# Kernel tuning notes

Measured on AMD Instinct MI355X. Metric: run time of the kernel, lower is better.

## Reference

```python
import jax, jax.numpy as jnp
import numpy as np
import math

HIDDEN = 1024
HEADS = 16
HEAD_DIM = HIDDEN // HEADS
B, S = 4, 2048


def setup_inputs() -> dict:
    key = jax.random.key(0)
    ks = jax.random.split(key, 10)
    x = jax.random.normal(ks[0], (B, S, HIDDEN), dtype=jnp.float32)
    time_intervals = jax.random.uniform(ks[1], (B, S, S), dtype=jnp.float32)
    mask = jax.random.randint(ks[2], (B, 1, S, S), 0, 2, dtype=jnp.int32)
    scale = 1.0 / math.sqrt(HIDDEN)
    Wq = jax.random.normal(ks[3], (HIDDEN, HIDDEN), dtype=jnp.float32) * scale
    bq = jnp.zeros((HIDDEN,), dtype=jnp.float32)
    Wk = jax.random.normal(ks[4], (HIDDEN, HIDDEN), dtype=jnp.float32) * scale
    bk = jnp.zeros((HIDDEN,), dtype=jnp.float32)
    Wv = jax.random.normal(ks[5], (HIDDEN, HIDDEN), dtype=jnp.float32) * scale
    bv = jnp.zeros((HIDDEN,), dtype=jnp.float32)
    alpha = jnp.asarray(0.1, dtype=jnp.float32)
    return {"x": x, "time_intervals": time_intervals, "mask": mask,
            "Wq": Wq, "bq": bq, "Wk": Wk, "bk": bk, "Wv": Wv, "bv": bv,
            "alpha": alpha}


def reference(x, time_intervals, mask, Wq, bq, Wk, bk, Wv, bv, alpha):
    b, s, _ = x.shape
    # projections -> [b, heads, s, head_dim]
    def proj(W, bias):
        y = x @ W + bias
        return y.reshape(b, s, HEADS, HEAD_DIM).transpose(0, 2, 1, 3)
    Q = proj(Wq, bq)
    K = proj(Wk, bk)
    V = proj(Wv, bv)
    scores = jnp.einsum('bhqd,bhkd->bhqk', Q, K) / math.sqrt(HEAD_DIM)
    # additive time-decay bias, broadcast over heads
    scores = scores + (-jnp.abs(alpha)) * time_intervals[:, None, :, :]
    scores = jnp.where(mask == 0, jnp.float32(-1e9), scores)
    attn = jax.nn.softmax(scores, axis=-1)
    out = jnp.einsum('bhqk,bhkd->bhqd', attn, V)
    return out.transpose(0, 2, 1, 3).reshape(b, s, HIDDEN)
```

## Files before the change

### kernel.cpp

```cpp
#include <hip/hip_runtime.h>
#include <hip/hip_bf16.h>
#include <hip/hip_fp16.h>

#define BATCH 4
#define SEQ   2048
#define HID   1024
#define HEADS 16
#define HDIM  64
#define MROWS (BATCH * SEQ)
#define LOG2E 1.4426950408889634f
#define SCL   (LOG2E / 8.0f)

typedef _Float16 v8h __attribute__((ext_vector_type(8)));
typedef _Float16 v4h __attribute__((ext_vector_type(4)));
typedef _Float16 v2h __attribute__((ext_vector_type(2)));
typedef float    v4f __attribute__((ext_vector_type(4)));
typedef int      v4i __attribute__((ext_vector_type(4)));

#define MFMA16(a, b, c) __builtin_amdgcn_mfma_f32_16x16x32_f16((a), (b), (c), 0, 0, 0)

__device__ inline int pk2(float a, float b) {
    return __builtin_bit_cast(int, __builtin_amdgcn_cvt_pkrtz(a, b));
}

__global__ __launch_bounds__(256) void cvt_x(const float* __restrict__ x,
                                             _Float16* __restrict__ xb) {
    int i = blockIdx.x * 256 + threadIdx.x;
    const float4* xp = (const float4*)x;
    float4 a = xp[2 * i];
    float4 b = xp[2 * i + 1];
    v4i o;
    o[0] = pk2(a.x, a.y); o[1] = pk2(a.z, a.w);
    o[2] = pk2(b.x, b.y); o[3] = pk2(b.z, b.w);
    ((v4i*)xb)[i] = o;
}

__global__ __launch_bounds__(256) void transw(const float* __restrict__ W,
                                              _Float16* __restrict__ Wt) {
    __shared__ float t[32][33];
    int bx = blockIdx.x * 32, by = blockIdx.y * 32;
    int tx = threadIdx.x, ty = threadIdx.y;
#pragma unroll
    for (int i = 0; i < 4; i++)
        t[ty + i * 8][tx] = W[(size_t)(by + ty + i * 8) * HID + bx + tx];
    __syncthreads();
#pragma unroll
    for (int i = 0; i < 4; i++)
        Wt[(size_t)(bx + ty + i * 8) * HID + by + tx] = (_Float16)t[tx][ty + i * 8];
}

__global__ __launch_bounds__(256) void mkbias(const float* __restrict__ tiv,
                                              const int* __restrict__ msk,
                                              const float* __restrict__ alphap,
                                              _Float16* __restrict__ biasT) {
    __shared__ _Float16 L[16 * 264];
    const int b = blockIdx.z, Q16 = blockIdx.y, kc0 = blockIdx.x * 256;
    const int tid = threadIdx.x;
    const float ca = -fabsf(alphap[0]) * LOG2E;
    const int prow = tid >> 6;
    const int pcol = (tid & 63) * 4;
#pragma unroll
    for (int pi = 0; pi < 4; pi++) {
        int r = pi * 4 + prow;
        size_t g = ((size_t)b * SEQ + Q16 * 16 + r) * SEQ + kc0 + pcol;
        float4 tv = *(const float4*)(tiv + g);
        int4   mv = *(const int4*)(msk + g);
        float f0 = mv.x ? ca * tv.x : -57344.0f;
        float f1 = mv.y ? ca * tv.y : -57344.0f;
        float f2 = mv.z ? ca * tv.z : -57344.0f;
        float f3 = mv.w ? ca * tv.w : -57344.0f;
        int2 o; o.x = pk2(f0, f1); o.y = pk2(f2, f3);
        *(int2*)&L[r * 264 + pcol] = o;
    }
    __syncthreads();
    const int lane = tid & 63, tq = tid >> 6;
#pragma unroll
    for (int it = 0; it < 4; it++) {
        int K16i = it * 4 + tq;
        int kl = K16i * 16 + (lane >> 4) * 4;
        int qr = lane & 15;
        int2 v = *(const int2*)&L[qr * 264 + kl];
        size_t o = ((((size_t)b * 128 + (kc0 >> 4) + K16i) * 128 + Q16) * 64 + lane) * 4;
        *(int2*)&biasT[o] = v;
    }
}

#define LDT 72

__global__ __launch_bounds__(256) void gemm_qkv(
    const _Float16* __restrict__ xb, const _Float16* __restrict__ wt,
    const float* __restrict__ bq, const float* __restrict__ bk,
    const float* __restrict__ bv,
    _Float16* __restrict__ Qb, _Float16* __restrict__ Kb, _Float16* __restrict__ Vtb) {
    const int mode = blockIdx.z;
    const _Float16* w = wt + (size_t)mode * HID * HID;
    __shared__ _Float16 As[128 * LDT];
    __shared__ _Float16 Bs[128 * LDT];
    const int tid = threadIdx.x;
    const int wv = tid >> 6, lane = tid & 63;
    const int quad = lane >> 4, l15 = lane & 15;
    const int wr = wv >> 1, wc = wv & 1;
    const int m0 = blockIdx.y * 128;
    const int n0 = blockIdx.x * 128;

    v4f acc[4][4];
#pragma unroll
    for (int i = 0; i < 4; i++)
#pragma unroll
        for (int j = 0; j < 4; j++) acc[i][j] = (v4f){0.f, 0.f, 0.f, 0.f};

    const int sr = tid >> 3;
    const int sc = (tid & 7) * 8;
    const _Float16* Ag = xb + (size_t)m0 * HID;
    const _Float16* Bg = w + (size_t)n0 * HID;

    for (int k0 = 0; k0 < HID; k0 += 64) {
        __syncthreads();
#pragma unroll
        for (int i = 0; i < 4; i++) {
            int r = sr + i * 32;
            *(uint4*)&As[r * LDT + sc] = *(const uint4*)&Ag[(size_t)r * HID + k0 + sc];
            *(uint4*)&Bs[r * LDT + sc] = *(const uint4*)&Bg[(size_t)r * HID + k0 + sc];
        }
        __syncthreads();
#pragma unroll
        for (int kc = 0; kc < 2; kc++) {
            v8h af[4], bf[4];
#pragma unroll
            for (int t = 0; t < 4; t++) {
                af[t] = *(const v8h*)&As[(wr * 64 + t * 16 + l15) * LDT + kc * 32 + quad * 8];
                bf[t] = *(const v8h*)&Bs[(wc * 64 + t * 16 + l15) * LDT + kc * 32 + quad * 8];
            }
#pragma unroll
            for (int tm = 0; tm < 4; tm++)
#pragma unroll
                for (int tn = 0; tn < 4; tn++)
                    acc[tm][tn] = MFMA16(af[tm], bf[tn], acc[tm][tn]);
        }
    }

    const float* pb = (mode == 0) ? bq : (mode == 1 ? bk : bv);
#pragma unroll
    for (int tm = 0; tm < 4; tm++) {
#pragma unroll
        for (int tn = 0; tn < 4; tn++) {
            int n = n0 + wc * 64 + tn * 16 + l15;
            float bval = pb[n];
            int h = n >> 6, d = n & 63;
#pragma unroll
            for (int r = 0; r < 4; r++) {
                int m = m0 + wr * 64 + tm * 16 + quad * 4 + r;
                int b = m >> 11, s = m & 2047;
                _Float16 hv = (_Float16)(acc[tm][tn][r] + bval);
                if (mode == 2) {
                    Vtb[(((size_t)(b * HEADS + h) * HDIM + d) * SEQ) + s] = hv;
                } else {
                    _Float16* dst = (mode == 0) ? Qb : Kb;
                    dst[((size_t)(b * HEADS + h) * SEQ + s) * HDIM + d] = hv;
                }
            }
        }
    }
}

__global__ __launch_bounds__(256, 4) void attn(
    const _Float16* __restrict__ Qb, const _Float16* __restrict__ Kb,
    const _Float16* __restrict__ Vtb, const _Float16* __restrict__ biasT,
    float* __restrict__ out) {
    const int bh = blockIdx.y;
    const int b = bh >> 4, h = bh & 15;
    const int qt = blockIdx.x;
    const int tid = threadIdx.x;
    const int wv = tid >> 6, lane = tid & 63;
    const int quad = lane >> 4, l15 = lane & 15;

    __shared__ _Float16 Ks[64 * LDT];
    __shared__ _Float16 Vs[64 * LDT];

    const int q0 = qt * 128 + wv * 32;
    const int Q16a = q0 >> 4;

    const _Float16* Qp = Qb + (size_t)(b * HEADS + h) * SEQ * HDIM;
    const _Float16* Kp = Kb + (size_t)(b * HEADS + h) * SEQ * HDIM;
    const _Float16* Vp = Vtb + (size_t)(b * HEADS + h) * HDIM * SEQ;
    const _Float16* Bbase = biasT + (size_t)b * 128 * 128 * 64 * 4;

    v8h qf[2][2];
#pragma unroll
    for (int tm = 0; tm < 2; tm++)
#pragma unroll
        for (int kc = 0; kc < 2; kc++)
            qf[tm][kc] = *(const v8h*)&Qp[(size_t)(q0 + tm * 16 + l15) * HDIM + kc * 32 + quad * 8];

    v4f oacc[2][4];
#pragma unroll
    for (int i = 0; i < 2; i++)
#pragma unroll
        for (int j = 0; j < 4; j++) oacc[i][j] = (v4f){0.f, 0.f, 0.f, 0.f};
    float lsum[2] = {0.f, 0.f};

    const int addrA = ((quad & 1) * 32 + l15) * 4;
    const int addrB = addrA + 64;
    const bool hiq = (quad >= 2);

    for (int kt = 0; kt < SEQ / 64; kt++) {
        const int key0 = kt * 64;
        int2 bld[4][2];
#pragma unroll
        for (int nt = 0; nt < 4; nt++)
#pragma unroll
            for (int tm = 0; tm < 2; tm++)
                bld[nt][tm] = *(const int2*)&Bbase[((((size_t)(key0 >> 4) + nt) * 128 + Q16a + tm) * 64 + lane) * 4];

        __syncthreads();
#pragma unroll
        for (int i = 0; i < 2; i++) {
            int idx = tid + 256 * i;
            int rr = idx >> 3, cc = (idx & 7) * 8;
            *(uint4*)&Ks[rr * LDT + cc] = *(const uint4*)&Kp[(size_t)(key0 + rr) * HDIM + cc];
            *(uint4*)&Vs[rr * LDT + cc] = *(const uint4*)&Vp[(size_t)rr * SEQ + key0 + cc];
        }
        __syncthreads();

        v4f sacc[4][2];
#pragma unroll
        for (int i = 0; i < 4; i++)
#pragma unroll
            for (int j = 0; j < 2; j++) sacc[i][j] = (v4f){0.f, 0.f, 0.f, 0.f};
#pragma unroll
        for (int kc = 0; kc < 2; kc++) {
            v8h kfr[4];
#pragma unroll
            for (int nt = 0; nt < 4; nt++)
                kfr[nt] = *(const v8h*)&Ks[(nt * 16 + l15) * LDT + kc * 32 + quad * 8];
#pragma unroll
            for (int nt = 0; nt < 4; nt++)
#pragma unroll
                for (int tm = 0; tm < 2; tm++)
                    sacc[nt][tm] = MFMA16(kfr[nt], qf[tm][kc], sacc[nt][tm]);
        }

        int pk[4][2][2];
#pragma unroll
        for (int nt = 0; nt < 4; nt++)
#pragma unroll
            for (int tm = 0; tm < 2; tm++) {
                v4h bv = __builtin_bit_cast(v4h, bld[nt][tm]);
                float p0 = __builtin_amdgcn_exp2f(sacc[nt][tm][0] * SCL + (float)bv[0]);
                float p1 = __builtin_amdgcn_exp2f(sacc[nt][tm][1] * SCL + (float)bv[1]);
                float p2 = __builtin_amdgcn_exp2f(sacc[nt][tm][2] * SCL + (float)bv[2]);
                float p3 = __builtin_amdgcn_exp2f(sacc[nt][tm][3] * SCL + (float)bv[3]);
                lsum[tm] += (p0 + p1) + (p2 + p3);
                pk[nt][tm][0] = pk2(p0, p1);
                pk[nt][tm][1] = pk2(p2, p3);
            }

        v8h pf[2][2];
#pragma unroll
        for (int kc = 0; kc < 2; kc++)
#pragma unroll
            for (int tm = 0; tm < 2; tm++) {
                int d0l = __builtin_amdgcn_ds_bpermute(addrA, pk[kc * 2][tm][0]);
                int d0h = __builtin_amdgcn_ds_bpermute(addrA, pk[kc * 2 + 1][tm][0]);
                int d1l = __builtin_amdgcn_ds_bpermute(addrA, pk[kc * 2][tm][1]);
                int d1h = __builtin_amdgcn_ds_bpermute(addrA, pk[kc * 2 + 1][tm][1]);
                int d2l = __builtin_amdgcn_ds_bpermute(addrB, pk[kc * 2][tm][0]);
                int d2h = __builtin_amdgcn_ds_bpermute(addrB, pk[kc * 2 + 1][tm][0]);
                int d3l = __builtin_amdgcn_ds_bpermute(addrB, pk[kc * 2][tm][1]);
                int d3h = __builtin_amdgcn_ds_bpermute(addrB, pk[kc * 2 + 1][tm][1]);
                v4i dw;
                dw[0] = hiq ? d0h : d0l;
                dw[1] = hiq ? d1h : d1l;
                dw[2] = hiq ? d2h : d2l;
                dw[3] = hiq ? d3h : d3l;
                pf[kc][tm] = __builtin_bit_cast(v8h, dw);
            }

#pragma unroll
        for (int kc = 0; kc < 2; kc++) {
            v8h vfr[4];
#pragma unroll
            for (int nt = 0; nt < 4; nt++)
                vfr[nt] = *(const v8h*)&Vs[(nt * 16 + l15) * LDT + kc * 32 + quad * 8];
#pragma unroll
            for (int tm = 0; tm < 2; tm++)
#pragma unroll
                for (int nt = 0; nt < 4; nt++)
                    oacc[tm][nt] = MFMA16(pf[kc][tm], vfr[nt], oacc[tm][nt]);
        }
    }

#pragma unroll
    for (int tm = 0; tm < 2; tm++) {
        float lt = lsum[tm];
        lt += __shfl_xor(lt, 16);
        lt += __shfl_xor(lt, 32);
        float inv[4];
#pragma unroll
        for (int r = 0; r < 4; r++)
            inv[r] = 1.0f / __shfl(lt, quad * 4 + r);
#pragma unroll
        for (int nt = 0; nt < 4; nt++)
#pragma unroll
            for (int r = 0; r < 4; r++) {
                int q = q0 + tm * 16 + quad * 4 + r;
                int d = nt * 16 + l15;
                out[((size_t)b * SEQ + q) * HID + h * HDIM + d] = oacc[tm][nt][r] * inv[r];
            }
    }
}

extern "C" void kernel_launch(void* const* d_in, const int* in_sizes, int n_in,
                              void* d_out, int out_size, void* d_ws, size_t ws_size,
                              hipStream_t stream) {
    const float* x    = (const float*)d_in[0];
    const float* tiv  = (const float*)d_in[1];
    const int*   msk  = (const int*)d_in[2];
    const float* Wq   = (const float*)d_in[3];
    const float* bq   = (const float*)d_in[4];
    const float* Wk   = (const float*)d_in[5];
    const float* bk   = (const float*)d_in[6];
    const float* Wv   = (const float*)d_in[7];
    const float* bv   = (const float*)d_in[8];
    const float* alp  = (const float*)d_in[9];

    char* ws = (char*)d_ws;
    const size_t XB_OFF = 0;
    const size_t WT_OFF = XB_OFF + (size_t)MROWS * HID * 2;
    const size_t Q_OFF  = WT_OFF + (size_t)3 * HID * HID * 2;
    const size_t K_OFF  = Q_OFF + (size_t)MROWS * HID * 2;
    const size_t V_OFF  = K_OFF + (size_t)MROWS * HID * 2;
    const size_t B_OFF  = V_OFF + (size_t)MROWS * HID * 2;

    _Float16* xb   = (_Float16*)(ws + XB_OFF);
    _Float16* wt   = (_Float16*)(ws + WT_OFF);
    _Float16* Qb   = (_Float16*)(ws + Q_OFF);
    _Float16* Kb   = (_Float16*)(ws + K_OFF);
    _Float16* Vtb  = (_Float16*)(ws + V_OFF);
    _Float16* bias = (_Float16*)(ws + B_OFF);

    cvt_x<<<MROWS * HID / (256 * 8), 256, 0, stream>>>(x, xb);
    dim3 tb(32, 8);
    transw<<<dim3(32, 32), tb, 0, stream>>>(Wq, wt);
    transw<<<dim3(32, 32), tb, 0, stream>>>(Wk, wt + HID * HID);
    transw<<<dim3(32, 32), tb, 0, stream>>>(Wv, wt + 2 * HID * HID);
    mkbias<<<dim3(SEQ / 256, SEQ / 16, BATCH), 256, 0, stream>>>(tiv, msk, alp, bias);
    gemm_qkv<<<dim3(HID / 128, MROWS / 128, 3), 256, 0, stream>>>(
        xb, wt, bq, bk, bv, Qb, Kb, Vtb);
    attn<<<dim3(SEQ / 128, BATCH * HEADS), 256, 0, stream>>>(Qb, Kb, Vtb, bias,
                                                             (float*)d_out);
}
```

Baseline: 436.1 us.

## Use async global-to-LDS loads with XOR swizzle and LDS-staged P in attention

Both the QKV GEMM and the attention kernel now load tiles with global_load_lds directly into XOR-swizzled, unpadded shared memory instead of staging through registers. Attention folds the softmax scale into Q at projection time and seeds the score accumulators with the bias, so the exponent needs no multiply-add. The probability tile is written to a per-wave LDS buffer instead of being shuffled with ds_bpermute, and the row sums use fdot2 on the packed fp16 values. This adds 16KB of LDS per block, which may reduce occupancy, and sums the rounded fp16 probabilities.

```diff
diff --git a/kernel.cpp b/kernel.cpp
--- a/kernel.cpp
+++ b/kernel.cpp
@@ -19,9 +19,23 @@
 
 #define MFMA16(a, b, c) __builtin_amdgcn_mfma_f32_16x16x32_f16((a), (b), (c), 0, 0, 0)
 
+#if __has_builtin(__builtin_amdgcn_fdot2)
+#define HAVE_FDOT2 1
+#else
+#define HAVE_FDOT2 0
+#endif
+
 __device__ inline int pk2(float a, float b) {
     return __builtin_bit_cast(int, __builtin_amdgcn_cvt_pkrtz(a, b));
 }
+
+__device__ __forceinline__ void async16(const void* g, void* l) {
+    __builtin_amdgcn_global_load_lds(
+        (const __attribute__((address_space(1))) unsigned int*)g,
+        (__attribute__((address_space(3))) unsigned int*)l, 16, 0, 0);
+}
+
+#define SWZ(row, chunk) (((row) * 64) + ((((chunk) ^ ((row) & 7))) * 8))
 
 __global__ __launch_bounds__(256) void cvt_x(const float* __restrict__ x,
                                              _Float16* __restrict__ xb) {
@@ -85,8 +99,6 @@
     }
 }
 
-#define LDT 72
-
 __global__ __launch_bounds__(256) void gemm_qkv(
     const _Float16* __restrict__ xb, const _Float16* __restrict__ wt,
     const float* __restrict__ bq, const float* __restrict__ bk,
@@ -94,8 +106,8 @@
     _Float16* __restrict__ Qb, _Float16* __restrict__ Kb, _Float16* __restrict__ Vtb) {
     const int mode = blockIdx.z;
     const _Float16* w = wt + (size_t)mode * HID * HID;
-    __shared__ _Float16 As[128 * LDT];
-    __shared__ _Float16 Bs[128 * LDT];
+    __shared__ _Float16 As[128 * 64];
+    __shared__ _Float16 Bs[128 * 64];
     const int tid = threadIdx.x;
     const int wv = tid >> 6, lane = tid & 63;
     const int quad = lane >> 4, l15 = lane & 15;
@@ -109,8 +121,8 @@
 #pragma unroll
         for (int j = 0; j < 4; j++) acc[i][j] = (v4f){0.f, 0.f, 0.f, 0.f};
 
-    const int sr = tid >> 3;
-    const int sc = (tid & 7) * 8;
+    const int srow = lane >> 3;
+    const int schk = lane & 7;
     const _Float16* Ag = xb + (size_t)m0 * HID;
     const _Float16* Bg = w + (size_t)n0 * HID;
 
@@ -118,9 +130,10 @@
         __syncthreads();
 #pragma unroll
         for (int i = 0; i < 4; i++) {
-            int r = sr + i * 32;
-            *(uint4*)&As[r * LDT + sc] = *(const uint4*)&Ag[(size_t)r * HID + k0 + sc];
-            *(uint4*)&Bs[r * LDT + sc] = *(const uint4*)&Bg[(size_t)r * HID + k0 + sc];
+            int ra = wv * 32 + i * 8 + srow;
+            int ca = schk ^ (ra & 7);
+            async16(Ag + (size_t)ra * HID + k0 + ca * 8, &As[(wv * 32 + i * 8) * 64]);
+            async16(Bg + (size_t)ra * HID + k0 + ca * 8, &Bs[(wv * 32 + i * 8) * 64]);
         }
         __syncthreads();
 #pragma unroll
@@ -128,8 +141,8 @@
             v8h af[4], bf[4];
 #pragma unroll
             for (int t = 0; t < 4; t++) {
-                af[t] = *(const v8h*)&As[(wr * 64 + t * 16 + l15) * LDT + kc * 32 + quad * 8];
-                bf[t] = *(const v8h*)&Bs[(wc * 64 + t * 16 + l15) * LDT + kc * 32 + quad * 8];
+                af[t] = *(const v8h*)&As[SWZ(wr * 64 + t * 16 + l15, kc * 4 + quad)];
+                bf[t] = *(const v8h*)&Bs[SWZ(wc * 64 + t * 16 + l15, kc * 4 + quad)];
             }
 #pragma unroll
             for (int tm = 0; tm < 4; tm++)
@@ -140,6 +153,7 @@
     }
 
     const float* pb = (mode == 0) ? bq : (mode == 1 ? bk : bv);
+    const float oscl = (mode == 0) ? SCL : 1.0f;
 #pragma unroll
     for (int tm = 0; tm < 4; tm++) {
 #pragma unroll
@@ -151,7 +165,7 @@
             for (int r = 0; r < 4; r++) {
                 int m = m0 + wr * 64 + tm * 16 + quad * 4 + r;
                 int b = m >> 11, s = m & 2047;
-                _Float16 hv = (_Float16)(acc[tm][tn][r] + bval);
+                _Float16 hv = (_Float16)((acc[tm][tn][r] + bval) * oscl);
                 if (mode == 2) {
                     Vtb[(((size_t)(b * HEADS + h) * HDIM + d) * SEQ) + s] = hv;
                 } else {
@@ -174,8 +188,9 @@
     const int wv = tid >> 6, lane = tid & 63;
     const int quad = lane >> 4, l15 = lane & 15;
 
-    __shared__ _Float16 Ks[64 * LDT];
-    __shared__ _Float16 Vs[64 * LDT];
+    __shared__ _Float16 Ks[64 * 64];
+    __shared__ _Float16 Vs[64 * 64];
+    __shared__ _Float16 Ps[4][32 * 64];
 
     const int q0 = qt * 128 + wv * 32;
     const int Q16a = q0 >> 4;
@@ -198,41 +213,40 @@
 #pragma unroll
         for (int j = 0; j < 4; j++) oacc[i][j] = (v4f){0.f, 0.f, 0.f, 0.f};
     float lsum[2] = {0.f, 0.f};
-
-    const int addrA = ((quad & 1) * 32 + l15) * 4;
-    const int addrB = addrA + 64;
-    const bool hiq = (quad >= 2);
+#if HAVE_FDOT2
+    const v2h one2 = {(_Float16)1.0f, (_Float16)1.0f};
+#endif
+
+    const int srow = lane >> 3, schk = lane & 7;
 
     for (int kt = 0; kt < SEQ / 64; kt++) {
         const int key0 = kt * 64;
-        int2 bld[4][2];
+        v4f sacc[4][2];
 #pragma unroll
         for (int nt = 0; nt < 4; nt++)
 #pragma unroll
-            for (int tm = 0; tm < 2; tm++)
-                bld[nt][tm] = *(const int2*)&Bbase[((((size_t)(key0 >> 4) + nt) * 128 + Q16a + tm) * 64 + lane) * 4];
+            for (int tm = 0; tm < 2; tm++) {
+                int2 bl = *(const int2*)&Bbase[((((size_t)(key0 >> 4) + nt) * 128 + Q16a + tm) * 64 + lane) * 4];
+                v4h bv = __builtin_bit_cast(v4h, bl);
+                sacc[nt][tm] = (v4f){(float)bv[0], (float)bv[1], (float)bv[2], (float)bv[3]};
+            }
 
         __syncthreads();
 #pragma unroll
         for (int i = 0; i < 2; i++) {
-            int idx = tid + 256 * i;
-            int rr = idx >> 3, cc = (idx & 7) * 8;
-            *(uint4*)&Ks[rr * LDT + cc] = *(const uint4*)&Kp[(size_t)(key0 + rr) * HDIM + cc];
-            *(uint4*)&Vs[rr * LDT + cc] = *(const uint4*)&Vp[(size_t)rr * SEQ + key0 + cc];
+            int r = wv * 16 + i * 8 + srow;
+            int c = schk ^ (r & 7);
+            async16(Kp + (size_t)(key0 + r) * HDIM + c * 8, &Ks[(wv * 16 + i * 8) * 64]);
+            async16(Vp + (size_t)r * SEQ + key0 + c * 8, &Vs[(wv * 16 + i * 8) * 64]);
         }
         __syncthreads();
 
-        v4f sacc[4][2];
-#pragma unroll
-        for (int i = 0; i < 4; i++)
-#pragma unroll
-            for (int j = 0; j < 2; j++) sacc[i][j] = (v4f){0.f, 0.f, 0.f, 0.f};
 #pragma unroll
         for (int kc = 0; kc < 2; kc++) {
             v8h kfr[4];
 #pragma unroll
             for (int nt = 0; nt < 4; nt++)
-                kfr[nt] = *(const v8h*)&Ks[(nt * 16 + l15) * LDT + kc * 32 + quad * 8];
+                kfr[nt] = *(const v8h*)&Ks[SWZ(nt * 16 + l15, kc * 4 + quad)];
 #pragma unroll
             for (int nt = 0; nt < 4; nt++)
 #pragma unroll
@@ -240,53 +254,42 @@
                     sacc[nt][tm] = MFMA16(kfr[nt], qf[tm][kc], sacc[nt][tm]);
         }
 
-        int pk[4][2][2];
 #pragma unroll
         for (int nt = 0; nt < 4; nt++)
 #pragma unroll
             for (int tm = 0; tm < 2; tm++) {
-                v4h bv = __builtin_bit_cast(v4h, bld[nt][tm]);
-                float p0 = __builtin_amdgcn_exp2f(sacc[nt][tm][0] * SCL + (float)bv[0]);
-                float p1 = __builtin_amdgcn_exp2f(sacc[nt][tm][1] * SCL + (float)bv[1]);
-                float p2 = __builtin_amdgcn_exp2f(sacc[nt][tm][2] * SCL + (float)bv[2]);
-                float p3 = __builtin_amdgcn_exp2f(sacc[nt][tm][3] * SCL + (float)bv[3]);
+                float p0 = __builtin_amdgcn_exp2f(sacc[nt][tm][0]);
+                float p1 = __builtin_amdgcn_exp2f(sacc[nt][tm][1]);
+                float p2 = __builtin_amdgcn_exp2f(sacc[nt][tm][2]);
+                float p3 = __builtin_amdgcn_exp2f(sacc[nt][tm][3]);
+                int2 pkv;
+                pkv.x = pk2(p0, p1);
+                pkv.y = pk2(p2, p3);
+#if HAVE_FDOT2
+                lsum[tm] = __builtin_amdgcn_fdot2(__builtin_bit_cast(v2h, pkv.x), one2, lsum[tm], false);
+                lsum[tm] = __builtin_amdgcn_fdot2(__builtin_bit_cast(v2h, pkv.y), one2, lsum[tm], false);
+#else
                 lsum[tm] += (p0 + p1) + (p2 + p3);
-                pk[nt][tm][0] = pk2(p0, p1);
-                pk[nt][tm][1] = pk2(p2, p3);
-            }
-
-        v8h pf[2][2];
-#pragma unroll
-        for (int kc = 0; kc < 2; kc++)
-#pragma unroll
-            for (int tm = 0; tm < 2; tm++) {
-                int d0l = __builtin_amdgcn_ds_bpermute(addrA, pk[kc * 2][tm][0]);
-                int d0h = __builtin_amdgcn_ds_bpermute(addrA, pk[kc * 2 + 1][tm][0]);
-                int d1l = __builtin_amdgcn_ds_bpermute(addrA, pk[kc * 2][tm][1]);
-                int d1h = __builtin_amdgcn_ds_bpermute(addrA, pk[kc * 2 + 1][tm][1]);
-                int d2l = __builtin_amdgcn_ds_bpermute(addrB, pk[kc * 2][tm][0]);
-                int d2h = __builtin_amdgcn_ds_bpermute(addrB, pk[kc * 2 + 1][tm][0]);
-                int d3l = __builtin_amdgcn_ds_bpermute(addrB, pk[kc * 2][tm][1]);
-                int d3h = __builtin_amdgcn_ds_bpermute(addrB, pk[kc * 2 + 1][tm][1]);
-                v4i dw;
-                dw[0] = hiq ? d0h : d0l;
-                dw[1] = hiq ? d1h : d1l;
-                dw[2] = hiq ? d2h : d2l;
-                dw[3] = hiq ? d3h : d3l;
-                pf[kc][tm] = __builtin_bit_cast(v8h, dw);
+#endif
+                int q = tm * 16 + l15;
+                int c16 = nt * 2 + (quad >> 1), half = quad & 1;
+                *(int2*)&Ps[wv][q * 64 + ((c16 ^ (q & 7)) * 8) + half * 4] = pkv;
             }
 
 #pragma unroll
         for (int kc = 0; kc < 2; kc++) {
-            v8h vfr[4];
+            v8h pf[2], vfr[4];
+#pragma unroll
+            for (int tm = 0; tm < 2; tm++)
+                pf[tm] = *(const v8h*)&Ps[wv][SWZ(tm * 16 + l15, kc * 4 + quad)];
 #pragma unroll
             for (int nt = 0; nt < 4; nt++)
-                vfr[nt] = *(const v8h*)&Vs[(nt * 16 + l15) * LDT + kc * 32 + quad * 8];
+                vfr[nt] = *(const v8h*)&Vs[SWZ(nt * 16 + l15, kc * 4 + quad)];
 #pragma unroll
             for (int tm = 0; tm < 2; tm++)
 #pragma unroll
                 for (int nt = 0; nt < 4; nt++)
-                    oacc[tm][nt] = MFMA16(pf[kc][tm], vfr[nt], oacc[tm][nt]);
+                    oacc[tm][nt] = MFMA16(pf[tm], vfr[nt], oacc[tm][nt]);
         }
     }
 
```

Result: faster. 393.0 us (-9.9%).
